# Performance work log

Measured on AMD Instinct MI355X. Metric: run time of the kernel, lower is better.

Reference implementation:

```python
import jax, jax.numpy as jnp
import numpy as np

SHIFT_RANGE = 8
LOSS_WEIGHT = 10.0
EPS = 1e-12


def _l2_normalize_rows(x):
    # matches F.normalize(x) on flattened rows: x / max(||x||_2, 1e-12)
    n = jnp.sqrt(jnp.sum(x * x, axis=1, keepdims=True))
    return x / jnp.maximum(n, EPS)


def _similarity(grd_feature, sat_feature):
    N, C, Hk, Wk = grd_feature.shape
    grd = _l2_normalize_rows(grd_feature.reshape(N, -1)).reshape(N, C, Hk, Wk)

    S = SHIFT_RANGE
    sat = jnp.pad(sat_feature, ((0, 0), (0, 0), (S, S), (S, S)))
    M, _, Hi, Wi = sat.shape
    sat = _l2_normalize_rows(sat.reshape(M, -1)).reshape(M, C, Hi, Wi)

    # all-pairs valid cross-correlation: corr[m,n,i,j] = sum_{c,h,w} sat[m,c,i+h,j+w]*grd[n,c,h,w]
    # lax.conv is cross-correlation, identical to the groups=N conv2d trick in torch.
    corr = jax.lax.conv_general_dilated(
        sat, grd, window_strides=(1, 1), padding='VALID',
        dimension_numbers=('NCHW', 'OIHW', 'NCHW'))  # [M, N, 2S+1, 2S+1]

    # avg_pool2d(sat^2, (Hk,Wk), stride=1, divisor_override=1) summed over channels
    energy = jnp.sum(sat * sat, axis=1)  # [M, Hi, Wi]
    partical = jax.lax.reduce_window(
        energy, 0.0, jax.lax.add, (1, Hk, Wk), (1, 1, 1), 'VALID')[:, None]  # [M,1,2S+1,2S+1]

    corr = corr / jnp.maximum(jnp.sqrt(partical), EPS)  # uncertainty = 1
    sim = jnp.max(corr, axis=(2, 3))  # [M, N]
    return sim


def _loss(sat_feature, grd_feature):
    B = grd_feature.shape[0]
    sim = _similarity(grd_feature, sat_feature)
    dist = 2.0 - 2.0 * sim  # [B, B], rows=sat, cols=grd
    pos = jnp.diagonal(dist)  # [B]
    pair_n = B * (B - 1)

    # log(1 + exp(x)) == softplus(x)
    loss_g2s = jnp.sum(jax.nn.softplus((pos[None, :] - dist) * LOSS_WEIGHT)) / pair_n
    loss_s2g = jnp.sum(jax.nn.softplus((pos[:, None] - dist) * LOSS_WEIGHT)) / pair_n
    loss = (loss_g2s + loss_s2g) / 2.0

    real_pos_dist_avg = jnp.mean(pos)
    pred_pos_dist_avg = jnp.mean(jnp.min(dist, axis=1))
    return 10.0 * loss, real_pos_dist_avg, pred_pos_dist_avg


def setup_inputs() -> dict:
    key = jax.random.key(0)
    k1, k2 = jax.random.split(key)
    sat_feature = jax.random.normal(k1, (16, 128, 64, 64), dtype=jnp.float32)
    grd_feature = jax.random.normal(k2, (16, 128, 64, 64), dtype=jnp.float32)
    return {"sat_feature": sat_feature, "grd_feature": grd_feature}


def reference(sat_feature, grd_feature):
    return _loss(sat_feature, grd_feature)
```

## Files before the change

kernel.cpp:

```cpp
#include <hip/hip_runtime.h>
#include <math.h>

#define CCH 128
#define HH 64
#define WW 64
#define SHD 17
#define NSHIFT (SHD*SHD)

#define OFF_KEY    0
#define OFF_NPART  256
#define OFF_EPART  8448
#define OFF_SCALE  532736
#define OFF_NORMS  537360
#define OFF_CNT    537376
#define OFF_SATP_B 2162688
#define SATP_SLICE_U16 (64*80*16*16)
#define OFF_GRDB_B (OFF_SATP_B + 8*SATP_SLICE_U16*2)
#define GRD_SLICE_U16 (64*64*16*16)
#define OFF_PART_B (OFF_GRDB_B + 8*GRD_SLICE_U16*2)
#define NBLK_CORR 1104

typedef __bf16 bf16x8 __attribute__((ext_vector_type(8)));
typedef float floatx4 __attribute__((ext_vector_type(4)));
typedef unsigned short ushort8 __attribute__((ext_vector_type(8)));

#define AS1 __attribute__((address_space(1)))
#define AS3 __attribute__((address_space(3)))

__device__ inline unsigned short f2bf(float f) {
    unsigned x = __float_as_uint(f);
    unsigned r = x + 0x7FFFu + ((x >> 16) & 1u);
    return (unsigned short)(r >> 16);
}

__global__ __launch_bounds__(256) void k_prep(const float* __restrict__ sat,
                                              const float* __restrict__ grd,
                                              float* __restrict__ ws) {
    __shared__ unsigned short tile[64 * 256];
    __shared__ float nred[16];
    int b = blockIdx.x;
    int tensor = b >> 9, h = (b >> 3) & 63, csl = b & 7;
    const float* src = tensor ? grd : sat;
    unsigned short* dstS = (unsigned short*)((char*)ws + OFF_SATP_B);
    unsigned short* dstG = (unsigned short*)((char*)ws + OFF_GRDB_B);
    int t = threadIdx.x;
    int n = t >> 4, wq = t & 15;

    float en0 = 0.f, en1 = 0.f, en2 = 0.f, en3 = 0.f;
    const float* base = src + ((size_t)(n * CCH + csl * 16) * 4096) + h * 64 + wq * 4;
    int w0 = wq * 4;
    #pragma unroll
    for (int c = 0; c < 16; ++c) {
        float4 v = *(const float4*)(base + (size_t)c * 4096);
        en0 = fmaf(v.x, v.x, en0); en1 = fmaf(v.y, v.y, en1);
        en2 = fmaf(v.z, v.z, en2); en3 = fmaf(v.w, v.w, en3);
        tile[(w0 + 0) * 256 + ((n + w0 + 0) & 15) * 16 + c] = f2bf(v.x);
        tile[(w0 + 1) * 256 + ((n + w0 + 1) & 15) * 16 + c] = f2bf(v.y);
        tile[(w0 + 2) * 256 + ((n + w0 + 2) & 15) * 16 + c] = f2bf(v.z);
        tile[(w0 + 3) * 256 + ((n + w0 + 3) & 15) * 16 + c] = f2bf(v.w);
    }

    if (tensor == 0) {
        float* eg = ws + OFF_EPART + (size_t)csl * 65536 + ((size_t)n * 64 + h) * 64 + w0;
        *(float4*)eg = make_float4(en0, en1, en2, en3);
    } else {
        float s = en0 + en1 + en2 + en3;
        #pragma unroll
        for (int off = 8; off; off >>= 1) s += __shfl_xor(s, off);
        if (wq == 0) nred[n] = s;
    }

    __syncthreads();
    if (tensor == 1 && t < 16)
        ws[OFF_NPART + (size_t)(h * 8 + csl) * 16 + t] = nred[t];

    unsigned short* dst = tensor
        ? dstG + (size_t)csl * GRD_SLICE_U16 + (size_t)h * 16384
        : dstS + (size_t)csl * SATP_SLICE_U16 + ((size_t)h * 80 + 8) * 256;
    #pragma unroll
    for (int i = 0; i < 8; ++i) {
        int o = i * 256 + t;
        int w = o >> 5, nn = (o >> 1) & 15, c8 = o & 1;
        ushort8 val = *(ushort8*)&tile[w * 256 + ((nn + w) & 15) * 16 + c8 * 8];
        *(ushort8*)&dst[(size_t)o * 8] = val;
    }
    if (tensor == 0) {
        ushort8 z = (ushort8)0;
        #pragma unroll
        for (int i = 0; i < 2; ++i) {
            int o = i * 256 + t;
            int slot = o >> 5, wi = o & 31;
            int ps = slot < 8 ? slot : slot + 64;
            *(ushort8*)&dstS[(size_t)csl * SATP_SLICE_U16 +
                             ((size_t)h * 80 + ps) * 256 + wi * 8] = z;
        }
    }
}

__global__ __launch_bounds__(256, 2) void k_corr(const unsigned short* __restrict__ satp,
                                                 const unsigned short* __restrict__ grdb,
                                                 float* __restrict__ part,
                                                 float* __restrict__ ws) {
    __shared__ alignas(16) unsigned char smem[81920];
    int b = blockIdx.x;
    int t = threadIdx.x;

    if (b >= 1088) {
        int m = b - 1088;
        float* E  = (float*)smem;
        float* R  = E + 4096;
        float* nr = R + 1088;
        if (t < 16) ((unsigned*)ws)[OFF_KEY + m * 16 + t] = 0u;
        if (m == 0 && t == 0) ((unsigned*)ws)[OFF_CNT] = 0u;
        float s = 0.f;
        for (int j = t; j < 512; j += 256) s += ws[OFF_NPART + (size_t)j * 16 + m];
        nr[t] = s; __syncthreads();
        for (int off = 128; off; off >>= 1) {
            if (t < off) nr[t] += nr[t + off];
            __syncthreads();
        }
        if (t == 0) ws[OFF_NORMS + m] = nr[0];
        const float* ep = ws + OFF_EPART + (size_t)m * 4096;
        for (int i = t; i < 4096; i += 256) {
            float e = 0.f;
            #pragma unroll
            for (int c = 0; c < 8; ++c) e += ep[(size_t)c * 65536 + i];
            E[i] = e;
        }
        __syncthreads();
        for (int i = t; i < 64 * 17; i += 256) {
            int y = i / 17, j = i % 17;
            int x0 = max(0, j - 8), x1 = min(64, j + 56);
            float e = 0.f;
            for (int x = x0; x < x1; ++x) e += E[y * 64 + x];
            R[i] = e;
        }
        __syncthreads();
        float* scale = ws + OFF_SCALE + (size_t)m * NSHIFT;
        for (int idx = t; idx < NSHIFT; idx += 256) {
            int ii = idx / 17, j = idx % 17;
            int y0 = max(0, ii - 8), y1 = min(64, ii + 56);
            float e = 0.f;
            for (int y = y0; y < y1; ++y) e += R[y * 17 + j];
            scale[idx] = 1.f / fmaxf(sqrtf(e), 1e-12f);
        }
        return;
    }

    int csl = b & 7;
    int r2  = b >> 3;
    int dyi = r2 % 17;
    int hq  = r2 / 17;
    int h0  = hq * 8;
    int wv = t >> 6, l = t & 63;
    int m16 = l & 15, q = l >> 4, jl = q >> 1, c8 = q & 1;
    int wbase = wv * 16;

    const unsigned short* sats = satp + (size_t)csl * SATP_SLICE_U16;
    const unsigned short* grds = grdb + (size_t)csl * GRD_SLICE_U16;
    const unsigned short* goff = grds + ((wbase + jl) * 16 + m16) * 16 + c8 * 8;
    int hl = max(0, 8 - dyi - h0), hu = min(8, 72 - dyi - h0);

    floatx4 acc[17];
    #pragma unroll
    for (int d = 0; d < 17; ++d) acc[d] = (floatx4)0.f;

    #define STAGE(hs, p)                                                            \
        do {                                                                        \
            _Pragma("unroll")                                                       \
            for (int i_ = 0; i_ < 10; ++i_) {                                       \
                const unsigned short* g_ = sats + (size_t)(hs) * 20480              \
                                         + wv * 5120 + i_ * 512 + l * 8;            \
                __builtin_amdgcn_global_load_lds((AS1 void*)(unsigned short*)g_,    \
                    (AS3 void*)(smem + (p) * 40960 + wv * 10240 + i_ * 1024 + l * 16), \
                    16, 0, 0);                                                      \
            }                                                                       \
        } while (0)

    if (hl < hu) {
        int hs0 = h0 + hl + dyi - 8;
        STAGE(hs0, 0);
        bf16x8 Bc[8], Bn[8];
        #pragma unroll
        for (int bi = 0; bi < 8; ++bi)
            Bc[bi] = *(const bf16x8*)(goff + (size_t)(h0 + hl) * 16384 + bi * 512);

        for (int hh = hl; hh < hu; ++hh) {
            __syncthreads();
            int p = (hh - hl) & 1;
            if (hh + 1 < hu) {
                STAGE(hs0 + (hh - hl) + 1, p ^ 1);
                #pragma unroll
                for (int bi = 0; bi < 8; ++bi)
                    Bn[bi] = *(const bf16x8*)(goff + (size_t)(h0 + hh + 1) * 16384 + bi * 512);
            }
            const unsigned char* aptr = smem + p * 40960 + jl * 512 + m16 * 32 + c8 * 16;
            bf16x8 A = *(const bf16x8*)(aptr + (size_t)wbase * 512);
            #pragma unroll
            for (int wo = 0; wo < 31; ++wo) {
                bf16x8 An = A;
                if (wo < 30) An = *(const bf16x8*)(aptr + (size_t)(wbase + wo + 1) * 512);
                #pragma unroll
                for (int bi = 0; bi < 8; ++bi) {
                    const int dxi = wo - 2 * bi;
                    if (dxi >= 0 && dxi <= 16)
                        acc[dxi] = __builtin_amdgcn_mfma_f32_16x16x32_bf16(A, Bc[bi], acc[dxi], 0, 0, 0);
                }
                A = An;
            }
            #pragma unroll
            for (int bi = 0; bi < 8; ++bi) Bc[bi] = Bn[bi];
        }
    }
    #undef STAGE

    __syncthreads();
    float* red = (float*)smem;
    #pragma unroll
    for (int dxi = 0; dxi < 17; ++dxi)
        #pragma unroll
        for (int r = 0; r < 4; ++r)
            red[(size_t)(wv * 68 + dxi * 4 + r) * 64 + l] = acc[dxi][r];
    __syncthreads();
    float* pw = part + (size_t)b * 4352;
    #pragma unroll
    for (int k = 0; k < 17; ++k) {
        int row = wv * 17 + k;
        float s = red[(size_t)(0 * 68 + row) * 64 + l]
                + red[(size_t)(1 * 68 + row) * 64 + l]
                + red[(size_t)(2 * 68 + row) * 64 + l]
                + red[(size_t)(3 * 68 + row) * 64 + l];
        pw[(size_t)row * 64 + l] = s;
    }
}

__global__ void k_reduce(const float* __restrict__ part, float* __restrict__ ws,
                         float* __restrict__ out) {
    int b = blockIdx.x;
    int dyi = b / 17, dxi = b % 17;
    int t = threadIdx.x;
    int l = t & 63, r = t >> 6;
    size_t eo = (size_t)(dxi * 4 + r) * 64 + l;
    float s = 0.f;
    for (int hq = 0; hq < 8; ++hq) {
        #pragma unroll
        for (int csl = 0; csl < 8; ++csl) {
            size_t blk = (size_t)((hq * 17 + dyi) * 8 + csl);
            s += part[blk * 4352 + eo];
        }
    }
    int n = l & 15, q = l >> 4, m = q * 4 + r;
    float val = s * ws[OFF_SCALE + m * NSHIFT + dyi * 17 + dxi];
    int iv = __float_as_int(val);
    unsigned key = (iv >= 0) ? ((unsigned)iv | 0x80000000u) : (unsigned)(~iv);
    atomicMax((unsigned*)ws + OFF_KEY + m * 16 + n, key);

    __shared__ unsigned done;
    __syncthreads();
    if (t == 0) {
        __threadfence();
        done = atomicAdd((unsigned*)ws + OFF_CNT, 1u);
    }
    __syncthreads();
    if (done != 288) return;
    __threadfence();

    __shared__ float dist_s[256];
    __shared__ float pos_s[16];
    __shared__ float red2[256];
    __shared__ float minv[16];
    unsigned u = atomicOr((unsigned*)ws + OFF_KEY + t, 0u);
    int iv2 = (u & 0x80000000u) ? (int)(u & 0x7fffffffu) : ~(int)u;
    float best = __int_as_float(iv2);
    int mm = t >> 4, nn = t & 15;
    float Ng  = sqrtf(ws[OFF_NORMS + nn]);
    float sim = best / fmaxf(Ng, 1e-12f);
    float d   = 2.f - 2.f * sim;
    dist_s[t] = d;
    if (mm == nn) pos_s[mm] = d;
    __syncthreads();

    float x1 = (pos_s[nn] - d) * 10.f;
    float x2 = (pos_s[mm] - d) * 10.f;
    float sp1 = x1 > 20.f ? x1 : log1pf(expf(x1));
    float sp2 = x2 > 20.f ? x2 : log1pf(expf(x2));
    red2[t] = sp1 + sp2;
    __syncthreads();
    for (int off = 128; off; off >>= 1) {
        if (t < off) red2[t] += red2[t + off];
        __syncthreads();
    }
    if (t < 16) {
        float mv = 1e30f;
        for (int k = 0; k < 16; ++k) mv = fminf(mv, dist_s[t * 16 + k]);
        minv[t] = mv;
    }
    __syncthreads();
    if (t == 0) {
        float psum = 0.f, msum = 0.f;
        for (int qq = 0; qq < 16; ++qq) { psum += pos_s[qq]; msum += minv[qq]; }
        out[0] = red2[0] / 48.f;
        out[1] = psum / 16.f;
        out[2] = msum / 16.f;
    }
}

extern "C" void kernel_launch(void* const* d_in, const int* in_sizes, int n_in,
                              void* d_out, int out_size, void* d_ws, size_t ws_size,
                              hipStream_t stream) {
    const float* sat = (const float*)d_in[0];
    const float* grd = (const float*)d_in[1];
    float* out = (float*)d_out;
    float* ws  = (float*)d_ws;
    const unsigned short* satp = (const unsigned short*)((char*)d_ws + OFF_SATP_B);
    const unsigned short* grdb = (const unsigned short*)((char*)d_ws + OFF_GRDB_B);
    float* part = (float*)((char*)d_ws + OFF_PART_B);

    k_prep  <<<1024,      256, 0, stream>>>(sat, grd, ws);
    k_corr  <<<NBLK_CORR, 256, 0, stream>>>(satp, grdb, part, ws);
    k_reduce<<<NSHIFT,    256, 0, stream>>>(part, ws, out);
}
```

Before: 178.8 us.

## Fuse prep, correlation and reduce into one persistent kernel with atomic work queues

Replaces three kernel launches with a single persistent kernel of 512 blocks that pulls work items from atomic counters and separates the prep, correlation and reduce phases with global spin barriers. It adds a hipMemsetAsync to reset the sync counters. The intent is to cut launch overhead and the inter-kernel tails. It risks deadlock if not all 512 blocks are co-resident, adds spin-wait cost, and moves the per-matrix scale computation into the csl-indexed queues.

```diff
diff --git a/kernel.cpp b/kernel.cpp
--- a/kernel.cpp
+++ b/kernel.cpp
@@ -12,13 +12,13 @@
 #define OFF_EPART  8448
 #define OFF_SCALE  532736
 #define OFF_NORMS  537360
-#define OFF_CNT    537376
+#define OFF_SYNC   537376
+#define OFF_SYNC_B 2149504
 #define OFF_SATP_B 2162688
 #define SATP_SLICE_U16 (64*80*16*16)
 #define OFF_GRDB_B (OFF_SATP_B + 8*SATP_SLICE_U16*2)
 #define GRD_SLICE_U16 (64*64*16*16)
 #define OFF_PART_B (OFF_GRDB_B + 8*GRD_SLICE_U16*2)
-#define NBLK_CORR 1104
 
 typedef __bf16 bf16x8 __attribute__((ext_vector_type(8)));
 typedef float floatx4 __attribute__((ext_vector_type(4)));
@@ -33,275 +33,304 @@
     return (unsigned short)(r >> 16);
 }
 
-__global__ __launch_bounds__(256) void k_prep(const float* __restrict__ sat,
-                                              const float* __restrict__ grd,
-                                              float* __restrict__ ws) {
-    __shared__ unsigned short tile[64 * 256];
-    __shared__ float nred[16];
-    int b = blockIdx.x;
-    int tensor = b >> 9, h = (b >> 3) & 63, csl = b & 7;
-    const float* src = tensor ? grd : sat;
-    unsigned short* dstS = (unsigned short*)((char*)ws + OFF_SATP_B);
-    unsigned short* dstG = (unsigned short*)((char*)ws + OFF_GRDB_B);
+__device__ inline void spin_ge(unsigned* c, unsigned tgt, int t) {
+    if (t == 0)
+        while (__hip_atomic_load(c, __ATOMIC_RELAXED, __HIP_MEMORY_SCOPE_AGENT) < tgt)
+            __builtin_amdgcn_s_sleep(2);
+    __syncthreads();
+    __threadfence();
+}
+
+__global__ __launch_bounds__(256, 2) void k_main(const float* __restrict__ sat,
+                                                 const float* __restrict__ grd,
+                                                 char* __restrict__ wsb,
+                                                 float* __restrict__ out) {
+    __shared__ alignas(16) unsigned char smem[81920];
+    unsigned* ubc = (unsigned*)(smem + 81912);
+    float* ws = (float*)wsb;
+    unsigned* sync = (unsigned*)wsb + OFF_SYNC;
+    unsigned short* satp_w = (unsigned short*)(wsb + OFF_SATP_B);
+    unsigned short* grdb_w = (unsigned short*)(wsb + OFF_GRDB_B);
+    float* part = (float*)(wsb + OFF_PART_B);
     int t = threadIdx.x;
-    int n = t >> 4, wq = t & 15;
-
-    float en0 = 0.f, en1 = 0.f, en2 = 0.f, en3 = 0.f;
-    const float* base = src + ((size_t)(n * CCH + csl * 16) * 4096) + h * 64 + wq * 4;
-    int w0 = wq * 4;
-    #pragma unroll
-    for (int c = 0; c < 16; ++c) {
-        float4 v = *(const float4*)(base + (size_t)c * 4096);
-        en0 = fmaf(v.x, v.x, en0); en1 = fmaf(v.y, v.y, en1);
-        en2 = fmaf(v.z, v.z, en2); en3 = fmaf(v.w, v.w, en3);
-        tile[(w0 + 0) * 256 + ((n + w0 + 0) & 15) * 16 + c] = f2bf(v.x);
-        tile[(w0 + 1) * 256 + ((n + w0 + 1) & 15) * 16 + c] = f2bf(v.y);
-        tile[(w0 + 2) * 256 + ((n + w0 + 2) & 15) * 16 + c] = f2bf(v.z);
-        tile[(w0 + 3) * 256 + ((n + w0 + 3) & 15) * 16 + c] = f2bf(v.w);
+    int bid = blockIdx.x;
+
+    for (;;) {
+        __syncthreads();
+        if (t == 0) *ubc = atomicAdd(&sync[0], 1u);
+        __syncthreads();
+        unsigned u = *ubc;
+        if (u >= 1024u) break;
+
+        int b = (int)u;
+        int tensor = b >> 9, h = (b >> 3) & 63, cslp = b & 7;
+        const float* src = tensor ? grd : sat;
+        unsigned short* tile = (unsigned short*)smem;
+        float* nredp = (float*)(smem + 32768);
+        int n = t >> 4, wq = t & 15;
+
+        float en0 = 0.f, en1 = 0.f, en2 = 0.f, en3 = 0.f;
+        const float* base = src + ((size_t)(n * CCH + cslp * 16) * 4096) + h * 64 + wq * 4;
+        int w0 = wq * 4;
+        #pragma unroll
+        for (int c = 0; c < 16; ++c) {
+            float4 v = *(const float4*)(base + (size_t)c * 4096);
+            en0 = fmaf(v.x, v.x, en0); en1 = fmaf(v.y, v.y, en1);
+            en2 = fmaf(v.z, v.z, en2); en3 = fmaf(v.w, v.w, en3);
+            tile[(w0 + 0) * 256 + ((n + w0 + 0) & 15) * 16 + c] = f2bf(v.x);
+            tile[(w0 + 1) * 256 + ((n + w0 + 1) & 15) * 16 + c] = f2bf(v.y);
+            tile[(w0 + 2) * 256 + ((n + w0 + 2) & 15) * 16 + c] = f2bf(v.z);
+            tile[(w0 + 3) * 256 + ((n + w0 + 3) & 15) * 16 + c] = f2bf(v.w);
+        }
+
+        if (tensor == 0) {
+            float* eg = ws + OFF_EPART + (size_t)cslp * 65536 + ((size_t)n * 64 + h) * 64 + w0;
+            *(float4*)eg = make_float4(en0, en1, en2, en3);
+        } else {
+            float s = en0 + en1 + en2 + en3;
+            #pragma unroll
+            for (int off = 8; off; off >>= 1) s += __shfl_xor(s, off);
+            if (wq == 0) nredp[n] = s;
+        }
+
+        __syncthreads();
+        if (tensor == 1 && t < 16)
+            ws[OFF_NPART + (size_t)(h * 8 + cslp) * 16 + t] = nredp[t];
+
+        unsigned short* dst = tensor
+            ? grdb_w + (size_t)cslp * GRD_SLICE_U16 + (size_t)h * 16384
+            : satp_w + (size_t)cslp * SATP_SLICE_U16 + ((size_t)h * 80 + 8) * 256;
+        #pragma unroll
+        for (int i = 0; i < 8; ++i) {
+            int o = i * 256 + t;
+            int w = o >> 5, nn = (o >> 1) & 15, c8 = o & 1;
+            ushort8 val = *(ushort8*)&tile[w * 256 + ((nn + w) & 15) * 16 + c8 * 8];
+            *(ushort8*)&dst[(size_t)o * 8] = val;
+        }
+        if (tensor == 0) {
+            ushort8 z = (ushort8)0;
+            #pragma unroll
+            for (int i = 0; i < 2; ++i) {
+                int o = i * 256 + t;
+                int slot = o >> 5, wi = o & 31;
+                int ps = slot < 8 ? slot : slot + 64;
+                *(ushort8*)&satp_w[(size_t)cslp * SATP_SLICE_U16 +
+                                   ((size_t)h * 80 + ps) * 256 + wi * 8] = z;
+            }
+        }
+        __threadfence();
+        __syncthreads();
+        if (t == 0) atomicAdd(&sync[1], 1u);
     }
-
-    if (tensor == 0) {
-        float* eg = ws + OFF_EPART + (size_t)csl * 65536 + ((size_t)n * 64 + h) * 64 + w0;
-        *(float4*)eg = make_float4(en0, en1, en2, en3);
-    } else {
-        float s = en0 + en1 + en2 + en3;
-        #pragma unroll
-        for (int off = 8; off; off >>= 1) s += __shfl_xor(s, off);
-        if (wq == 0) nred[n] = s;
-    }
-
-    __syncthreads();
-    if (tensor == 1 && t < 16)
-        ws[OFF_NPART + (size_t)(h * 8 + csl) * 16 + t] = nred[t];
-
-    unsigned short* dst = tensor
-        ? dstG + (size_t)csl * GRD_SLICE_U16 + (size_t)h * 16384
-        : dstS + (size_t)csl * SATP_SLICE_U16 + ((size_t)h * 80 + 8) * 256;
-    #pragma unroll
-    for (int i = 0; i < 8; ++i) {
-        int o = i * 256 + t;
-        int w = o >> 5, nn = (o >> 1) & 15, c8 = o & 1;
-        ushort8 val = *(ushort8*)&tile[w * 256 + ((nn + w) & 15) * 16 + c8 * 8];
-        *(ushort8*)&dst[(size_t)o * 8] = val;
-    }
-    if (tensor == 0) {
-        ushort8 z = (ushort8)0;
-        #pragma unroll
-        for (int i = 0; i < 2; ++i) {
-            int o = i * 256 + t;
-            int slot = o >> 5, wi = o & 31;
-            int ps = slot < 8 ? slot : slot + 64;
-            *(ushort8*)&dstS[(size_t)csl * SATP_SLICE_U16 +
-                             ((size_t)h * 80 + ps) * 256 + wi * 8] = z;
-        }
-    }
-}
-
-__global__ __launch_bounds__(256, 2) void k_corr(const unsigned short* __restrict__ satp,
-                                                 const unsigned short* __restrict__ grdb,
-                                                 float* __restrict__ part,
-                                                 float* __restrict__ ws) {
-    __shared__ alignas(16) unsigned char smem[81920];
-    int b = blockIdx.x;
-    int t = threadIdx.x;
-
-    if (b >= 1088) {
-        int m = b - 1088;
-        float* E  = (float*)smem;
-        float* R  = E + 4096;
-        float* nr = R + 1088;
-        if (t < 16) ((unsigned*)ws)[OFF_KEY + m * 16 + t] = 0u;
-        if (m == 0 && t == 0) ((unsigned*)ws)[OFF_CNT] = 0u;
-        float s = 0.f;
-        for (int j = t; j < 512; j += 256) s += ws[OFF_NPART + (size_t)j * 16 + m];
-        nr[t] = s; __syncthreads();
-        for (int off = 128; off; off >>= 1) {
-            if (t < off) nr[t] += nr[t + off];
-            __syncthreads();
-        }
-        if (t == 0) ws[OFF_NORMS + m] = nr[0];
-        const float* ep = ws + OFF_EPART + (size_t)m * 4096;
-        for (int i = t; i < 4096; i += 256) {
-            float e = 0.f;
-            #pragma unroll
-            for (int c = 0; c < 8; ++c) e += ep[(size_t)c * 65536 + i];
-            E[i] = e;
-        }
-        __syncthreads();
-        for (int i = t; i < 64 * 17; i += 256) {
-            int y = i / 17, j = i % 17;
-            int x0 = max(0, j - 8), x1 = min(64, j + 56);
-            float e = 0.f;
-            for (int x = x0; x < x1; ++x) e += E[y * 64 + x];
-            R[i] = e;
-        }
-        __syncthreads();
-        float* scale = ws + OFF_SCALE + (size_t)m * NSHIFT;
-        for (int idx = t; idx < NSHIFT; idx += 256) {
-            int ii = idx / 17, j = idx % 17;
-            int y0 = max(0, ii - 8), y1 = min(64, ii + 56);
-            float e = 0.f;
-            for (int y = y0; y < y1; ++y) e += R[y * 17 + j];
-            scale[idx] = 1.f / fmaxf(sqrtf(e), 1e-12f);
-        }
-        return;
-    }
-
-    int csl = b & 7;
-    int r2  = b >> 3;
-    int dyi = r2 % 17;
-    int hq  = r2 / 17;
-    int h0  = hq * 8;
-    int wv = t >> 6, l = t & 63;
-    int m16 = l & 15, q = l >> 4, jl = q >> 1, c8 = q & 1;
-    int wbase = wv * 16;
-
-    const unsigned short* sats = satp + (size_t)csl * SATP_SLICE_U16;
-    const unsigned short* grds = grdb + (size_t)csl * GRD_SLICE_U16;
-    const unsigned short* goff = grds + ((wbase + jl) * 16 + m16) * 16 + c8 * 8;
-    int hl = max(0, 8 - dyi - h0), hu = min(8, 72 - dyi - h0);
-
-    floatx4 acc[17];
-    #pragma unroll
-    for (int d = 0; d < 17; ++d) acc[d] = (floatx4)0.f;
-
-    #define STAGE(hs, p)                                                            \
-        do {                                                                        \
-            _Pragma("unroll")                                                       \
-            for (int i_ = 0; i_ < 10; ++i_) {                                       \
-                const unsigned short* g_ = sats + (size_t)(hs) * 20480              \
-                                         + wv * 5120 + i_ * 512 + l * 8;            \
-                __builtin_amdgcn_global_load_lds((AS1 void*)(unsigned short*)g_,    \
-                    (AS3 void*)(smem + (p) * 40960 + wv * 10240 + i_ * 1024 + l * 16), \
-                    16, 0, 0);                                                      \
-            }                                                                       \
-        } while (0)
-
-    if (hl < hu) {
-        int hs0 = h0 + hl + dyi - 8;
-        STAGE(hs0, 0);
-        bf16x8 Bc[8], Bn[8];
-        #pragma unroll
-        for (int bi = 0; bi < 8; ++bi)
-            Bc[bi] = *(const bf16x8*)(goff + (size_t)(h0 + hl) * 16384 + bi * 512);
-
-        for (int hh = hl; hh < hu; ++hh) {
-            __syncthreads();
-            int p = (hh - hl) & 1;
-            if (hh + 1 < hu) {
-                STAGE(hs0 + (hh - hl) + 1, p ^ 1);
+    spin_ge(&sync[1], 1024u, t);
+
+    int csl = bid & 7;
+    const unsigned short* sats = satp_w + (size_t)csl * SATP_SLICE_U16;
+    const unsigned short* grds = grdb_w + (size_t)csl * GRD_SLICE_U16;
+    for (;;) {
+        __syncthreads();
+        if (t == 0) *ubc = atomicAdd(&sync[4 + csl], 1u);
+        __syncthreads();
+        unsigned u = *ubc;
+        if (u >= 138u) break;
+
+        if (u < 2u) {
+            int m = csl + 8 * (int)u;
+            float* E  = (float*)smem;
+            float* R  = E + 4096;
+            float* nr = R + 1088;
+            if (t < 16) ((unsigned*)ws)[OFF_KEY + m * 16 + t] = 0u;
+            float s = 0.f;
+            for (int j = t; j < 512; j += 256) s += ws[OFF_NPART + (size_t)j * 16 + m];
+            nr[t] = s; __syncthreads();
+            for (int off = 128; off; off >>= 1) {
+                if (t < off) nr[t] += nr[t + off];
+                __syncthreads();
+            }
+            if (t == 0) ws[OFF_NORMS + m] = nr[0];
+            const float* ep = ws + OFF_EPART + (size_t)m * 4096;
+            for (int i = t; i < 4096; i += 256) {
+                float e = 0.f;
+                #pragma unroll
+                for (int c = 0; c < 8; ++c) e += ep[(size_t)c * 65536 + i];
+                E[i] = e;
+            }
+            __syncthreads();
+            for (int i = t; i < 64 * 17; i += 256) {
+                int y = i / 17, j = i % 17;
+                int x0 = max(0, j - 8), x1 = min(64, j + 56);
+                float e = 0.f;
+                for (int x = x0; x < x1; ++x) e += E[y * 64 + x];
+                R[i] = e;
+            }
+            __syncthreads();
+            float* scale = ws + OFF_SCALE + (size_t)m * NSHIFT;
+            for (int idx = t; idx < NSHIFT; idx += 256) {
+                int ii = idx / 17, j = idx % 17;
+                int y0 = max(0, ii - 8), y1 = min(64, ii + 56);
+                float e = 0.f;
+                for (int y = y0; y < y1; ++y) e += R[y * 17 + j];
+                scale[idx] = 1.f / fmaxf(sqrtf(e), 1e-12f);
+            }
+        } else {
+            int r2  = (int)u - 2;
+            int dyi = r2 % 17;
+            int hq  = r2 / 17;
+            int h0  = hq * 8;
+            int wv = t >> 6, l = t & 63;
+            int m16 = l & 15, q = l >> 4, jl = q >> 1, c8 = q & 1;
+            int wbase = wv * 16;
+            const unsigned short* goff = grds + ((wbase + jl) * 16 + m16) * 16 + c8 * 8;
+            int hl = max(0, 8 - dyi - h0), hu = min(8, 72 - dyi - h0);
+
+            floatx4 acc[17];
+            #pragma unroll
+            for (int d = 0; d < 17; ++d) acc[d] = (floatx4)0.f;
+
+            #define STAGE(hs, p)                                                        \
+                do {                                                                    \
+                    _Pragma("unroll")                                                   \
+                    for (int i_ = 0; i_ < 10; ++i_) {                                   \
+                        const unsigned short* g_ = sats + (size_t)(hs) * 20480          \
+                                                 + wv * 5120 + i_ * 512 + l * 8;        \
+                        __builtin_amdgcn_global_load_lds((AS1 void*)(unsigned short*)g_,\
+                            (AS3 void*)(smem + (p) * 40960 + wv * 10240 + i_ * 1024 + l * 16), \
+                            16, 0, 0);                                                  \
+                    }                                                                   \
+                } while (0)
+
+            if (hl < hu) {
+                int hs0 = h0 + hl + dyi - 8;
+                STAGE(hs0, 0);
+                bf16x8 Bc[8], Bn[8];
                 #pragma unroll
                 for (int bi = 0; bi < 8; ++bi)
-                    Bn[bi] = *(const bf16x8*)(goff + (size_t)(h0 + hh + 1) * 16384 + bi * 512);
-            }
-            const unsigned char* aptr = smem + p * 40960 + jl * 512 + m16 * 32 + c8 * 16;
-            bf16x8 A = *(const bf16x8*)(aptr + (size_t)wbase * 512);
-            #pragma unroll
-            for (int wo = 0; wo < 31; ++wo) {
-                bf16x8 An = A;
-                if (wo < 30) An = *(const bf16x8*)(aptr + (size_t)(wbase + wo + 1) * 512);
+                    Bc[bi] = *(const bf16x8*)(goff + (size_t)(h0 + hl) * 16384 + bi * 512);
+
+                for (int hh = hl; hh < hu; ++hh) {
+                    __syncthreads();
+                    int p = (hh - hl) & 1;
+                    if (hh + 1 < hu) {
+                        STAGE(hs0 + (hh - hl) + 1, p ^ 1);
+                        #pragma unroll
+                        for (int bi = 0; bi < 8; ++bi)
+                            Bn[bi] = *(const bf16x8*)(goff + (size_t)(h0 + hh + 1) * 16384 + bi * 512);
+                    }
+                    const unsigned char* aptr = smem + p * 40960 + jl * 512 + m16 * 32 + c8 * 16;
+                    bf16x8 A = *(const bf16x8*)(aptr + (size_t)wbase * 512);
+                    #pragma unroll
+                    for (int wo = 0; wo < 31; ++wo) {
+                        bf16x8 An = A;
+                        if (wo < 30) An = *(const bf16x8*)(aptr + (size_t)(wbase + wo + 1) * 512);
+                        #pragma unroll
+                        for (int bi = 0; bi < 8; ++bi) {
+                            const int dxi = wo - 2 * bi;
+                            if (dxi >= 0 && dxi <= 16)
+                                acc[dxi] = __builtin_amdgcn_mfma_f32_16x16x32_bf16(A, Bc[bi], acc[dxi], 0, 0, 0);
+                        }
+                        A = An;
+                    }
+                    #pragma unroll
+                    for (int bi = 0; bi < 8; ++bi) Bc[bi] = Bn[bi];
+                }
+            }
+            #undef STAGE
+
+            __syncthreads();
+            float* red = (float*)smem;
+            #pragma unroll
+            for (int dxi = 0; dxi < 17; ++dxi)
                 #pragma unroll
-                for (int bi = 0; bi < 8; ++bi) {
-                    const int dxi = wo - 2 * bi;
-                    if (dxi >= 0 && dxi <= 16)
-                        acc[dxi] = __builtin_amdgcn_mfma_f32_16x16x32_bf16(A, Bc[bi], acc[dxi], 0, 0, 0);
-                }
-                A = An;
-            }
-            #pragma unroll
-            for (int bi = 0; bi < 8; ++bi) Bc[bi] = Bn[bi];
-        }
+                for (int r = 0; r < 4; ++r)
+                    red[(size_t)(wv * 68 + dxi * 4 + r) * 64 + l] = acc[dxi][r];
+            __syncthreads();
+            float* pw = part + (size_t)(r2 * 8 + csl) * 4352;
+            #pragma unroll
+            for (int k = 0; k < 17; ++k) {
+                int row = wv * 17 + k;
+                float s = red[(size_t)(0 * 68 + row) * 64 + l]
+                        + red[(size_t)(1 * 68 + row) * 64 + l]
+                        + red[(size_t)(2 * 68 + row) * 64 + l]
+                        + red[(size_t)(3 * 68 + row) * 64 + l];
+                pw[(size_t)row * 64 + l] = s;
+            }
+        }
+        __threadfence();
+        __syncthreads();
+        if (t == 0) atomicAdd(&sync[3], 1u);
     }
-    #undef STAGE
-
-    __syncthreads();
-    float* red = (float*)smem;
-    #pragma unroll
-    for (int dxi = 0; dxi < 17; ++dxi)
-        #pragma unroll
-        for (int r = 0; r < 4; ++r)
-            red[(size_t)(wv * 68 + dxi * 4 + r) * 64 + l] = acc[dxi][r];
-    __syncthreads();
-    float* pw = part + (size_t)b * 4352;
-    #pragma unroll
-    for (int k = 0; k < 17; ++k) {
-        int row = wv * 17 + k;
-        float s = red[(size_t)(0 * 68 + row) * 64 + l]
-                + red[(size_t)(1 * 68 + row) * 64 + l]
-                + red[(size_t)(2 * 68 + row) * 64 + l]
-                + red[(size_t)(3 * 68 + row) * 64 + l];
-        pw[(size_t)row * 64 + l] = s;
-    }
-}
-
-__global__ void k_reduce(const float* __restrict__ part, float* __restrict__ ws,
-                         float* __restrict__ out) {
-    int b = blockIdx.x;
-    int dyi = b / 17, dxi = b % 17;
-    int t = threadIdx.x;
-    int l = t & 63, r = t >> 6;
-    size_t eo = (size_t)(dxi * 4 + r) * 64 + l;
-    float s = 0.f;
-    for (int hq = 0; hq < 8; ++hq) {
-        #pragma unroll
-        for (int csl = 0; csl < 8; ++csl) {
-            size_t blk = (size_t)((hq * 17 + dyi) * 8 + csl);
-            s += part[blk * 4352 + eo];
-        }
-    }
-    int n = l & 15, q = l >> 4, m = q * 4 + r;
-    float val = s * ws[OFF_SCALE + m * NSHIFT + dyi * 17 + dxi];
-    int iv = __float_as_int(val);
-    unsigned key = (iv >= 0) ? ((unsigned)iv | 0x80000000u) : (unsigned)(~iv);
-    atomicMax((unsigned*)ws + OFF_KEY + m * 16 + n, key);
-
-    __shared__ unsigned done;
-    __syncthreads();
-    if (t == 0) {
-        __threadfence();
-        done = atomicAdd((unsigned*)ws + OFF_CNT, 1u);
-    }
-    __syncthreads();
-    if (done != 288) return;
-    __threadfence();
-
-    __shared__ float dist_s[256];
-    __shared__ float pos_s[16];
-    __shared__ float red2[256];
-    __shared__ float minv[16];
-    unsigned u = atomicOr((unsigned*)ws + OFF_KEY + t, 0u);
-    int iv2 = (u & 0x80000000u) ? (int)(u & 0x7fffffffu) : ~(int)u;
-    float best = __int_as_float(iv2);
-    int mm = t >> 4, nn = t & 15;
-    float Ng  = sqrtf(ws[OFF_NORMS + nn]);
-    float sim = best / fmaxf(Ng, 1e-12f);
-    float d   = 2.f - 2.f * sim;
-    dist_s[t] = d;
-    if (mm == nn) pos_s[mm] = d;
-    __syncthreads();
-
-    float x1 = (pos_s[nn] - d) * 10.f;
-    float x2 = (pos_s[mm] - d) * 10.f;
-    float sp1 = x1 > 20.f ? x1 : log1pf(expf(x1));
-    float sp2 = x2 > 20.f ? x2 : log1pf(expf(x2));
-    red2[t] = sp1 + sp2;
-    __syncthreads();
-    for (int off = 128; off; off >>= 1) {
-        if (t < off) red2[t] += red2[t + off];
-        __syncthreads();
-    }
-    if (t < 16) {
-        float mv = 1e30f;
-        for (int k = 0; k < 16; ++k) mv = fminf(mv, dist_s[t * 16 + k]);
-        minv[t] = mv;
-    }
-    __syncthreads();
-    if (t == 0) {
-        float psum = 0.f, msum = 0.f;
-        for (int qq = 0; qq < 16; ++qq) { psum += pos_s[qq]; msum += minv[qq]; }
-        out[0] = red2[0] / 48.f;
-        out[1] = psum / 16.f;
-        out[2] = msum / 16.f;
+    spin_ge(&sync[3], 1104u, t);
+
+    for (;;) {
+        __syncthreads();
+        if (t == 0) *ubc = atomicAdd(&sync[2], 1u);
+        __syncthreads();
+        unsigned u = *ubc;
+        if (u >= 289u) break;
+
+        int dyi = (int)u / 17, dxi = (int)u % 17;
+        int l = t & 63, r = t >> 6;
+        size_t eo = (size_t)(dxi * 4 + r) * 64 + l;
+        float s = 0.f;
+        for (int hq = 0; hq < 8; ++hq) {
+            #pragma unroll
+            for (int c = 0; c < 8; ++c) {
+                size_t blk = (size_t)((hq * 17 + dyi) * 8 + c);
+                s += part[blk * 4352 + eo];
+            }
+        }
+        int n = l & 15, q = l >> 4, m = q * 4 + r;
+        float val = s * ws[OFF_SCALE + m * NSHIFT + dyi * 17 + dxi];
+        int iv = __float_as_int(val);
+        unsigned key = (iv >= 0) ? ((unsigned)iv | 0x80000000u) : (unsigned)(~iv);
+        atomicMax((unsigned*)ws + OFF_KEY + m * 16 + n, key);
+
+        unsigned* dflag = (unsigned*)smem;
+        __syncthreads();
+        if (t == 0) { __threadfence(); *dflag = atomicAdd(&sync[12], 1u); }
+        __syncthreads();
+        bool last = (*dflag == 288u);
+        __syncthreads();
+        if (!last) continue;
+
+        float* dist_s = (float*)(smem + 16);
+        float* pos_s  = dist_s + 256;
+        float* red2   = pos_s + 16;
+        float* minv   = red2 + 256;
+        unsigned uk = atomicOr((unsigned*)ws + OFF_KEY + t, 0u);
+        int iv2 = (uk & 0x80000000u) ? (int)(uk & 0x7fffffffu) : ~(int)uk;
+        float best = __int_as_float(iv2);
+        int mm = t >> 4, nn = t & 15;
+        float Ng  = sqrtf(ws[OFF_NORMS + nn]);
+        float sim = best / fmaxf(Ng, 1e-12f);
+        float d   = 2.f - 2.f * sim;
+        dist_s[t] = d;
+        if (mm == nn) pos_s[mm] = d;
+        __syncthreads();
+
+        float x1 = (pos_s[nn] - d) * 10.f;
+        float x2 = (pos_s[mm] - d) * 10.f;
+        float sp1 = x1 > 20.f ? x1 : log1pf(expf(x1));
+        float sp2 = x2 > 20.f ? x2 : log1pf(expf(x2));
+        red2[t] = sp1 + sp2;
+        __syncthreads();
+        for (int off = 128; off; off >>= 1) {
+            if (t < off) red2[t] += red2[t + off];
+            __syncthreads();
+        }
+        if (t < 16) {
+            float mv = 1e30f;
+            for (int k = 0; k < 16; ++k) mv = fminf(mv, dist_s[t * 16 + k]);
+            minv[t] = mv;
+        }
+        __syncthreads();
+        if (t == 0) {
+            float psum = 0.f, msum = 0.f;
+            for (int qq = 0; qq < 16; ++qq) { psum += pos_s[qq]; msum += minv[qq]; }
+            out[0] = red2[0] / 48.f;
+            out[1] = psum / 16.f;
+            out[2] = msum / 16.f;
+        }
     }
 }
 
@@ -311,12 +340,7 @@
     const float* sat = (const float*)d_in[0];
     const float* grd = (const float*)d_in[1];
     float* out = (float*)d_out;
-    float* ws  = (float*)d_ws;
-    const unsigned short* satp = (const unsigned short*)((char*)d_ws + OFF_SATP_B);
-    const unsigned short* grdb = (const unsigned short*)((char*)d_ws + OFF_GRDB_B);
-    float* part = (float*)((char*)d_ws + OFF_PART_B);
-
-    k_prep  <<<1024,      256, 0, stream>>>(sat, grd, ws);
-    k_corr  <<<NBLK_CORR, 256, 0, stream>>>(satp, grdb, part, ws);
-    k_reduce<<<NSHIFT,    256, 0, stream>>>(part, ws, out);
+
+    hipMemsetAsync((char*)d_ws + OFF_SYNC_B, 0, 64, stream);
+    k_main<<<512, 256, 0, stream>>>(sat, grd, (char*)d_ws, out);
 }
```

Measured after the change: 544.9 us. +204.7%, slower.
